# Optimization experiments

Measured on AMD Instinct MI355X. Metric: run time of the kernel, lower is better.

## Reference

```python
import jax, jax.numpy as jnp
import numpy as np

NUM_TOKENS = 16384
MODEL_DIM = 4096
MAX_EXPERTS = 128
INITIAL_EXPERTS = 64
THRESHOLD = 0.5  # rm_threshold


def setup_inputs() -> dict:
    key = jax.random.key(0)
    k1, k2 = jax.random.split(key)
    x = jax.random.normal(k1, (NUM_TOKENS, MODEL_DIM), dtype=jnp.float32)
    # Linear(model_dim, max_expert_num, bias=False).weight -> [E_max, D]
    wg_weight = jax.random.normal(k2, (MAX_EXPERTS, MODEL_DIM), dtype=jnp.float32) * (1.0 / np.sqrt(MODEL_DIM))
    # experts_mask: first `INITIAL_EXPERTS` active
    experts_mask = (jnp.arange(MAX_EXPERTS) < INITIAL_EXPERTS).astype(jnp.float32)
    return {"x": x, "wg_weight": wg_weight, "experts_mask": experts_mask}


def reference(x, wg_weight, experts_mask):
    # gate logits: [N, E_max]
    scores = jnp.einsum("nd,ed->ne", x, wg_weight)
    # mask inactive experts
    scores = jnp.where(experts_mask[None, :] == 0, jnp.float32(-1e9), scores)
    # fp32 softmax + epsilon (matches F.softmax(..., dtype=float32) + 1e-14)
    scores = jax.nn.softmax(scores.astype(jnp.float32), axis=-1) + 1e-14
    # sort descending along expert dim
    sorted_scores = -jnp.sort(-scores, axis=-1)
    cum_scores = jnp.cumsum(sorted_scores, axis=-1)
    # adaptive top-k: experts needed to accumulate THRESHOLD routing mass
    mask = (cum_scores - sorted_scores) < THRESHOLD
    top_k = mask.sum(axis=-1).astype(jnp.int32)
    active_experts = experts_mask.sum().astype(jnp.int32)
    top_k = jnp.minimum(top_k, active_experts)
    return scores.astype(x.dtype), top_k
```

## Files before the change

kernel.cpp:

```cpp
#include <hip/hip_runtime.h>
#include <hip/hip_bf16.h>
#include <stdint.h>

#define NTOK 16384
#define DDIM 4096
#define NEXP 128
#define BM 32
#define BK 64
#define NT (DDIM / BK)

typedef __attribute__((ext_vector_type(8))) short short8;
typedef __attribute__((ext_vector_type(4))) float f32x4;
typedef __attribute__((address_space(1))) const uint32_t gu32;
typedef __attribute__((address_space(3))) uint32_t lu32;

__device__ __forceinline__ void gload16(const void* g, void* l) {
    __builtin_amdgcn_global_load_lds((gu32*)g, (lu32*)l, 16, 0, 0);
}

__device__ __forceinline__ void split_bf16(float f, uint32_t& h, uint32_t& l) {
    uint32_t u = __float_as_uint(f);
    h = (u + 0x7FFFu + ((u >> 16) & 1u)) >> 16;
    float r = f - __uint_as_float(h << 16);
    uint32_t v = __float_as_uint(r);
    l = (v + 0x7FFFu + ((v >> 16) & 1u)) >> 16;
}

__global__ void prep_w(const float* __restrict__ w,
                       uint16_t* __restrict__ whi, uint16_t* __restrict__ wlo) {
    int i = (blockIdx.x * blockDim.x + threadIdx.x) * 4;
    float4 f = *(const float4*)(w + i);
    uint32_t h0, h1, h2, h3, l0, l1, l2, l3;
    split_bf16(f.x, h0, l0);
    split_bf16(f.y, h1, l1);
    split_bf16(f.z, h2, l2);
    split_bf16(f.w, h3, l3);
    uint2 hv = make_uint2(h0 | (h1 << 16), h2 | (h3 << 16));
    uint2 lv = make_uint2(l0 | (l1 << 16), l2 | (l3 << 16));
    *(uint2*)(whi + i) = hv;
    *(uint2*)(wlo + i) = lv;
}

__global__ __launch_bounds__(256) void gemm_logits(
    const float* __restrict__ x,
    const uint16_t* __restrict__ whi, const uint16_t* __restrict__ wlo,
    float* __restrict__ S)
{
    __shared__ uint16_t sAh[2][BM * BK], sAl[2][BM * BK];
    __shared__ uint16_t sBh[2][NEXP * BK], sBl[2][NEXP * BK];

    const int tid  = threadIdx.x;
    const int lane = tid & 63;
    const int wave = tid >> 6;
    const int q = lane >> 4;
    const int c = lane & 15;
    const int rxor = c & 7;
    const int m0 = blockIdx.x * BM;

    const int ar = tid >> 3, aj = tid & 7;
    const float* xp = x + (size_t)(m0 + ar) * DDIM + aj * 8;
    const int aoff = ar * BK + (aj ^ (ar & 7)) * 8;

    const int bjj = aj ^ (ar & 7);
    const size_t bgo = (size_t)ar * DDIM + bjj * 8;
    const int bd = tid * 8;

    f32x4 acc[2][2];
    #pragma unroll
    for (int mt = 0; mt < 2; ++mt)
        #pragma unroll
        for (int nt = 0; nt < 2; ++nt)
            acc[mt][nt] = (f32x4){0.f, 0.f, 0.f, 0.f};

    auto stageB = [&](int nxt, int kn) {
        #pragma unroll
        for (int rr = 0; rr < 4; ++rr) {
            const size_t go = bgo + (size_t)rr * 32 * DDIM + kn;
            gload16(whi + go, &sBh[nxt][bd + rr * 2048]);
            gload16(wlo + go, &sBl[nxt][bd + rr * 2048]);
        }
    };

    auto writeA = [&](int nxt, float4 fa, float4 fb) {
        uint32_t h[8], l[8];
        split_bf16(fa.x, h[0], l[0]); split_bf16(fa.y, h[1], l[1]);
        split_bf16(fa.z, h[2], l[2]); split_bf16(fa.w, h[3], l[3]);
        split_bf16(fb.x, h[4], l[4]); split_bf16(fb.y, h[5], l[5]);
        split_bf16(fb.z, h[6], l[6]); split_bf16(fb.w, h[7], l[7]);
        uint4 hv = make_uint4(h[0] | (h[1] << 16), h[2] | (h[3] << 16),
                              h[4] | (h[5] << 16), h[6] | (h[7] << 16));
        uint4 lv = make_uint4(l[0] | (l[1] << 16), l[2] | (l[3] << 16),
                              l[4] | (l[5] << 16), l[6] | (l[7] << 16));
        *(uint4*)&sAh[nxt][aoff] = hv;
        *(uint4*)&sAl[nxt][aoff] = lv;
    };

    auto compute = [&](int cur) {
        #pragma unroll
        for (int ks = 0; ks < 2; ++ks) {
            const int off = (((ks << 2) | q) ^ rxor) << 3;
            short8 ah[2], alo[2], bh[2], blo[2];
            #pragma unroll
            for (int mt = 0; mt < 2; ++mt) {
                const int ro = (mt * 16 + c) * BK + off;
                ah[mt]  = *(const short8*)&sAh[cur][ro];
                alo[mt] = *(const short8*)&sAl[cur][ro];
            }
            #pragma unroll
            for (int nt = 0; nt < 2; ++nt) {
                const int ro = (wave * 32 + nt * 16 + c) * BK + off;
                bh[nt]  = *(const short8*)&sBh[cur][ro];
                blo[nt] = *(const short8*)&sBl[cur][ro];
            }
            #pragma unroll
            for (int mt = 0; mt < 2; ++mt)
                #pragma unroll
                for (int nt = 0; nt < 2; ++nt) {
                    acc[mt][nt] = __builtin_amdgcn_mfma_f32_16x16x32_bf16(alo[mt], bh[nt],  acc[mt][nt], 0, 0, 0);
                    acc[mt][nt] = __builtin_amdgcn_mfma_f32_16x16x32_bf16(ah[mt],  blo[nt], acc[mt][nt], 0, 0, 0);
                    acc[mt][nt] = __builtin_amdgcn_mfma_f32_16x16x32_bf16(ah[mt],  bh[nt],  acc[mt][nt], 0, 0, 0);
                }
        }
    };

    stageB(0, 0);
    {
        float4 fa = *(const float4*)(xp);
        float4 fb = *(const float4*)(xp + 4);
        writeA(0, fa, fb);
    }
    __syncthreads();

    #pragma unroll 2
    for (int t = 0; t < NT - 1; ++t) {
        const int cur = t & 1, nxt = cur ^ 1;
        const int kn = (t + 1) * BK;
        stageB(nxt, kn);
        float4 fa = *(const float4*)(xp + kn);
        float4 fb = *(const float4*)(xp + kn + 4);
        compute(cur);
        writeA(nxt, fa, fb);
        __syncthreads();
    }
    compute((NT - 1) & 1);

    #pragma unroll
    for (int mt = 0; mt < 2; ++mt)
        #pragma unroll
        for (int nt = 0; nt < 2; ++nt) {
            const int e = wave * 32 + nt * 16 + c;
            #pragma unroll
            for (int r = 0; r < 4; ++r) {
                const int tok = m0 + mt * 16 + q * 4 + r;
                S[(size_t)tok * NEXP + e] = acc[mt][nt][r];
            }
        }
}

__global__ __launch_bounds__(256) void postproc(
    float* __restrict__ S, const float* __restrict__ mask,
    float* __restrict__ topk_out)
{
    const int lane = threadIdx.x & 63;
    const int wave = threadIdx.x >> 6;
    const int g  = lane >> 4;
    const int gl = lane & 15;
    const int tok = blockIdx.x * 16 + wave * 4 + g;
    float* row = S + (size_t)tok * NEXP;

    float v[8];
    bool act[8];
    int cnt = 0;
    #pragma unroll
    for (int j = 0; j < 8; ++j) {
        v[j] = row[gl + 16 * j];
        act[j] = (mask[gl + 16 * j] != 0.f);
        cnt += act[j] ? 1 : 0;
    }
    int active = cnt;
    #pragma unroll
    for (int off = 8; off; off >>= 1) active += __shfl_xor(active, off);

    float mx = -3.0e38f;
    #pragma unroll
    for (int j = 0; j < 8; ++j) mx = fmaxf(mx, act[j] ? v[j] : -3.0e38f);
    #pragma unroll
    for (int off = 8; off; off >>= 1) mx = fmaxf(mx, __shfl_xor(mx, off));

    float sum = 0.f;
    #pragma unroll
    for (int j = 0; j < 8; ++j) {
        v[j] = act[j] ? __expf(v[j] - mx) : 0.f;
        sum += v[j];
    }
    #pragma unroll
    for (int off = 8; off; off >>= 1) sum += __shfl_xor(sum, off);

    const float inv = 1.0f / sum;
    #pragma unroll
    for (int j = 0; j < 8; ++j) {
        v[j] = v[j] * inv + 1e-14f;
        row[gl + 16 * j] = v[j];
    }

    float cum = 0.f;
    int k = 0;
    bool done = false;
    while (__ballot(!done)) {
        if (!done) {
            float mv = v[0];
            #pragma unroll
            for (int j = 1; j < 8; ++j) mv = fmaxf(mv, v[j]);
            #pragma unroll
            for (int off = 8; off; off >>= 1) mv = fmaxf(mv, __shfl_xor(mv, off));
            cum += mv;
            ++k;
            bool has = false;
            #pragma unroll
            for (int j = 0; j < 8; ++j) has |= (v[j] == mv);
            unsigned int m16 = (unsigned int)((__ballot(has) >> (g * 16)) & 0xFFFFull);
            int first = __ffs(m16) - 1;
            if (gl == first) {
                bool cleared = false;
                #pragma unroll
                for (int j = 0; j < 8; ++j) {
                    if (!cleared && v[j] == mv) { v[j] = -1.f; cleared = true; }
                }
            }
            done = (cum >= 0.5f) || (k >= NEXP);
        }
    }
    int topk = k < active ? k : active;
    if (gl == 0) topk_out[tok] = (float)topk;
}

extern "C" void kernel_launch(void* const* d_in, const int* in_sizes, int n_in,
                              void* d_out, int out_size, void* d_ws, size_t ws_size,
                              hipStream_t stream) {
    (void)in_sizes; (void)n_in; (void)out_size; (void)ws_size;
    const float* x    = (const float*)d_in[0];
    const float* w    = (const float*)d_in[1];
    const float* mask = (const float*)d_in[2];

    float* S    = (float*)d_out;
    float* topk = S + (size_t)NTOK * NEXP;

    uint16_t* whi = (uint16_t*)d_ws;
    uint16_t* wlo = whi + (size_t)NEXP * DDIM;

    hipLaunchKernelGGL(prep_w, dim3((NEXP * DDIM) / (256 * 4)), dim3(256), 0, stream,
                       w, whi, wlo);
    hipLaunchKernelGGL(gemm_logits, dim3(NTOK / BM), dim3(256), 0, stream,
                       x, whi, wlo, S);
    hipLaunchKernelGGL(postproc, dim3(NTOK / 16), dim3(256), 0, stream,
                       S, mask, topk);
}
```

Measured before the change: 425.8 us.

## Load raw fp32 x via async LDS loads and deepen the pipeline to 4 stages

The GEMM now stages raw fp32 x tiles straight into LDS with global_load_lds instead of loading into registers, splitting into bf16 hi/lo and writing LDS. The hi/lo split moves to the compute phase, after the LDS read. The K-tile shrinks to 32 and the double buffer becomes a 4-deep ring, synchronised with explicit vmcnt waits and barriers, and the kernel asks for 2 blocks per CU. The aim is to keep more memory traffic in flight and drop register-staged A stores. The cost is a repeated split per wave (each wave re-splits A), more barriers per K, and reliance on hand-counted vmcnt values; the last iterations also re-stage redundant tiles.

Measured after the change: 475.0 us. 1.12x slower.

```diff
diff --git a/kernel.cpp b/kernel.cpp
--- a/kernel.cpp
+++ b/kernel.cpp
@@ -6,8 +6,9 @@
 #define DDIM 4096
 #define NEXP 128
 #define BM 32
-#define BK 64
+#define BK 32
 #define NT (DDIM / BK)
+#define NBUF 4
 
 typedef __attribute__((ext_vector_type(8))) short short8;
 typedef __attribute__((ext_vector_type(4))) float f32x4;
@@ -41,29 +42,32 @@
     *(uint2*)(wlo + i) = lv;
 }
 
-__global__ __launch_bounds__(256) void gemm_logits(
+__global__ __launch_bounds__(256, 2) void gemm_logits(
     const float* __restrict__ x,
     const uint16_t* __restrict__ whi, const uint16_t* __restrict__ wlo,
     float* __restrict__ S)
 {
-    __shared__ uint16_t sAh[2][BM * BK], sAl[2][BM * BK];
-    __shared__ uint16_t sBh[2][NEXP * BK], sBl[2][NEXP * BK];
+    __shared__ float    sA[NBUF * BM * BK];
+    __shared__ uint16_t sBh[NBUF * NEXP * BK];
+    __shared__ uint16_t sBl[NBUF * NEXP * BK];
 
     const int tid  = threadIdx.x;
     const int lane = tid & 63;
     const int wave = tid >> 6;
     const int q = lane >> 4;
     const int c = lane & 15;
-    const int rxor = c & 7;
     const int m0 = blockIdx.x * BM;
 
-    const int ar = tid >> 3, aj = tid & 7;
-    const float* xp = x + (size_t)(m0 + ar) * DDIM + aj * 8;
-    const int aoff = ar * BK + (aj ^ (ar & 7)) * 8;
-
-    const int bjj = aj ^ (ar & 7);
-    const size_t bgo = (size_t)ar * DDIM + bjj * 8;
-    const int bd = tid * 8;
+    const int ar = tid >> 3;
+    const int ajj = (tid & 7) ^ (ar & 7);
+    const float* xsrc = x + (size_t)(m0 + ar) * DDIM + ajj * 4;
+    const int adst = tid * 4;
+
+    const int br  = tid >> 2;
+    const int bslot = tid & 3;
+    const int bx  = (br & 3) ^ ((br >> 2) & 1);
+    const size_t bsrc = (size_t)br * DDIM + (size_t)(bslot ^ bx) * 8;
+    const int bdst0 = tid * 8, bdst1 = (tid + 256) * 8;
 
     f32x4 acc[2][2];
     #pragma unroll
@@ -72,77 +76,68 @@
         for (int nt = 0; nt < 2; ++nt)
             acc[mt][nt] = (f32x4){0.f, 0.f, 0.f, 0.f};
 
-    auto stageB = [&](int nxt, int kn) {
-        #pragma unroll
-        for (int rr = 0; rr < 4; ++rr) {
-            const size_t go = bgo + (size_t)rr * 32 * DDIM + kn;
-            gload16(whi + go, &sBh[nxt][bd + rr * 2048]);
-            gload16(wlo + go, &sBl[nxt][bd + rr * 2048]);
-        }
+    auto stage = [&](int bi, int kt) {
+        const int kk = kt * BK;
+        gload16(xsrc + kk, &sA[bi * BM * BK + adst]);
+        gload16(whi + bsrc + kk, &sBh[bi * NEXP * BK + bdst0]);
+        gload16(whi + bsrc + (size_t)64 * DDIM + kk, &sBh[bi * NEXP * BK + bdst1]);
+        gload16(wlo + bsrc + kk, &sBl[bi * NEXP * BK + bdst0]);
+        gload16(wlo + bsrc + (size_t)64 * DDIM + kk, &sBl[bi * NEXP * BK + bdst1]);
     };
 
-    auto writeA = [&](int nxt, float4 fa, float4 fb) {
-        uint32_t h[8], l[8];
-        split_bf16(fa.x, h[0], l[0]); split_bf16(fa.y, h[1], l[1]);
-        split_bf16(fa.z, h[2], l[2]); split_bf16(fa.w, h[3], l[3]);
-        split_bf16(fb.x, h[4], l[4]); split_bf16(fb.y, h[5], l[5]);
-        split_bf16(fb.z, h[6], l[6]); split_bf16(fb.w, h[7], l[7]);
-        uint4 hv = make_uint4(h[0] | (h[1] << 16), h[2] | (h[3] << 16),
-                              h[4] | (h[5] << 16), h[6] | (h[7] << 16));
-        uint4 lv = make_uint4(l[0] | (l[1] << 16), l[2] | (l[3] << 16),
-                              l[4] | (l[5] << 16), l[6] | (l[7] << 16));
-        *(uint4*)&sAh[nxt][aoff] = hv;
-        *(uint4*)&sAl[nxt][aoff] = lv;
+    auto compute = [&](int bi) {
+        const float* A = &sA[bi * BM * BK];
+        const uint16_t* Bh = &sBh[bi * NEXP * BK];
+        const uint16_t* Bl = &sBl[bi * NEXP * BK];
+        short8 ah[2], al[2], bh[2], bl[2];
+        #pragma unroll
+        for (int mt = 0; mt < 2; ++mt) {
+            const int row = mt * 16 + c;
+            const int rb = row * BK;
+            const float4 x0 = *(const float4*)&A[rb + ((((q << 1)    ) ^ (row & 7)) << 2)];
+            const float4 x1 = *(const float4*)&A[rb + ((((q << 1) | 1) ^ (row & 7)) << 2)];
+            const float f[8] = {x0.x, x0.y, x0.z, x0.w, x1.x, x1.y, x1.z, x1.w};
+            short8 hv, lv;
+            #pragma unroll
+            for (int j = 0; j < 8; ++j) {
+                uint32_t hh, ll;
+                split_bf16(f[j], hh, ll);
+                hv[j] = (short)hh;
+                lv[j] = (short)ll;
+            }
+            ah[mt] = hv;
+            al[mt] = lv;
+        }
+        #pragma unroll
+        for (int nt = 0; nt < 2; ++nt) {
+            const int row = wave * 32 + nt * 16 + c;
+            const int slot = q ^ ((row & 3) ^ ((row >> 2) & 1));
+            const int off = row * BK + slot * 8;
+            bh[nt] = *(const short8*)&Bh[off];
+            bl[nt] = *(const short8*)&Bl[off];
+        }
+        #pragma unroll
+        for (int mt = 0; mt < 2; ++mt)
+            #pragma unroll
+            for (int nt = 0; nt < 2; ++nt) {
+                acc[mt][nt] = __builtin_amdgcn_mfma_f32_16x16x32_bf16(al[mt], bh[nt], acc[mt][nt], 0, 0, 0);
+                acc[mt][nt] = __builtin_amdgcn_mfma_f32_16x16x32_bf16(ah[mt], bl[nt], acc[mt][nt], 0, 0, 0);
+                acc[mt][nt] = __builtin_amdgcn_mfma_f32_16x16x32_bf16(ah[mt], bh[nt], acc[mt][nt], 0, 0, 0);
+            }
     };
 
-    auto compute = [&](int cur) {
-        #pragma unroll
-        for (int ks = 0; ks < 2; ++ks) {
-            const int off = (((ks << 2) | q) ^ rxor) << 3;
-            short8 ah[2], alo[2], bh[2], blo[2];
-            #pragma unroll
-            for (int mt = 0; mt < 2; ++mt) {
-                const int ro = (mt * 16 + c) * BK + off;
-                ah[mt]  = *(const short8*)&sAh[cur][ro];
-                alo[mt] = *(const short8*)&sAl[cur][ro];
-            }
-            #pragma unroll
-            for (int nt = 0; nt < 2; ++nt) {
-                const int ro = (wave * 32 + nt * 16 + c) * BK + off;
-                bh[nt]  = *(const short8*)&sBh[cur][ro];
-                blo[nt] = *(const short8*)&sBl[cur][ro];
-            }
-            #pragma unroll
-            for (int mt = 0; mt < 2; ++mt)
-                #pragma unroll
-                for (int nt = 0; nt < 2; ++nt) {
-                    acc[mt][nt] = __builtin_amdgcn_mfma_f32_16x16x32_bf16(alo[mt], bh[nt],  acc[mt][nt], 0, 0, 0);
-                    acc[mt][nt] = __builtin_amdgcn_mfma_f32_16x16x32_bf16(ah[mt],  blo[nt], acc[mt][nt], 0, 0, 0);
-                    acc[mt][nt] = __builtin_amdgcn_mfma_f32_16x16x32_bf16(ah[mt],  bh[nt],  acc[mt][nt], 0, 0, 0);
-                }
-        }
-    };
-
-    stageB(0, 0);
-    {
-        float4 fa = *(const float4*)(xp);
-        float4 fb = *(const float4*)(xp + 4);
-        writeA(0, fa, fb);
-    }
-    __syncthreads();
-
-    #pragma unroll 2
-    for (int t = 0; t < NT - 1; ++t) {
-        const int cur = t & 1, nxt = cur ^ 1;
-        const int kn = (t + 1) * BK;
-        stageB(nxt, kn);
-        float4 fa = *(const float4*)(xp + kn);
-        float4 fb = *(const float4*)(xp + kn + 4);
-        compute(cur);
-        writeA(nxt, fa, fb);
-        __syncthreads();
-    }
-    compute((NT - 1) & 1);
+    stage(0, 0);
+    stage(1, 1);
+    stage(2, 2);
+    asm volatile("s_waitcnt vmcnt(10) lgkmcnt(0)\n\ts_barrier" ::: "memory");
+
+    #pragma unroll 4
+    for (int t = 0; t < NT; ++t) {
+        const int ts = (t + 3 < NT) ? t + 3 : NT - 1;
+        stage((t + 3) & 3, ts);
+        compute(t & 3);
+        asm volatile("s_waitcnt vmcnt(10) lgkmcnt(0)\n\ts_barrier" ::: "memory");
+    }
 
     #pragma unroll
     for (int mt = 0; mt < 2; ++mt)
```
